# Kernel tuning notes

Hardware: AMD Instinct MI355X
Metric: run time of the kernel (lower is better)

Reference implementation:

```python
import jax, jax.numpy as jnp
import numpy as np

D_MODEL = 1024
N_HEADS = 16
D_FF = 4 * D_MODEL
EPS = 1e-5


def _layer_norm(x, g, b):
    mu = jnp.mean(x, axis=-1, keepdims=True)
    var = jnp.mean(jnp.square(x - mu), axis=-1, keepdims=True)
    return (x - mu) * jax.lax.rsqrt(var + EPS) * g + b


def _mha(x, Wq, Wk, Wv, Wo, causal):
    B, S, D = x.shape
    H = N_HEADS
    Dh = D // H
    q = (x @ Wq).reshape(B, S, H, Dh)
    k = (x @ Wk).reshape(B, S, H, Dh)
    v = (x @ Wv).reshape(B, S, H, Dh)
    scores = jnp.einsum('bqhd,bkhd->bhqk', q, k) / jnp.sqrt(jnp.asarray(Dh, x.dtype))
    if causal:
        mask = jnp.tril(jnp.ones((S, S), dtype=bool))  # [S,S] causal mask
        scores = jnp.where(mask, scores, jnp.asarray(-1e9, x.dtype))
    attn = jax.nn.softmax(scores, axis=-1)
    out = jnp.einsum('bhqk,bkhd->bqhd', attn, v).reshape(B, S, D)
    return out @ Wo


def _ffn(x, W1, b1, W2, b2):
    return jax.nn.relu(x @ W1 + b1) @ W2 + b2


def setup_inputs() -> dict:
    key = jax.random.key(0)
    ks = jax.random.split(key, 12)
    sd = 1.0 / np.sqrt(D_MODEL)
    sf = 1.0 / np.sqrt(D_FF)
    B, S = 4, 1024
    return {
        'X': jax.random.normal(ks[0], (B, S, D_MODEL), jnp.float32),
        'Wq1': jax.random.normal(ks[1], (D_MODEL, D_MODEL), jnp.float32) * sd,
        'Wk1': jax.random.normal(ks[2], (D_MODEL, D_MODEL), jnp.float32) * sd,
        'Wv1': jax.random.normal(ks[3], (D_MODEL, D_MODEL), jnp.float32) * sd,
        'Wo1': jax.random.normal(ks[4], (D_MODEL, D_MODEL), jnp.float32) * sd,
        'Wq2': jax.random.normal(ks[5], (D_MODEL, D_MODEL), jnp.float32) * sd,
        'Wk2': jax.random.normal(ks[6], (D_MODEL, D_MODEL), jnp.float32) * sd,
        'Wv2': jax.random.normal(ks[7], (D_MODEL, D_MODEL), jnp.float32) * sd,
        'Wo2': jax.random.normal(ks[8], (D_MODEL, D_MODEL), jnp.float32) * sd,
        'ln_g': jnp.ones((D_MODEL,), jnp.float32),
        'ln_b': jnp.zeros((D_MODEL,), jnp.float32),
        'W1': jax.random.normal(ks[9], (D_MODEL, D_FF), jnp.float32) * sd,
        'b1': jnp.zeros((D_FF,), jnp.float32),
        'W2': jax.random.normal(ks[10], (D_FF, D_MODEL), jnp.float32) * sf,
        'b2': jnp.zeros((D_MODEL,), jnp.float32),
    }


def reference(X, Wq1, Wk1, Wv1, Wo1, Wq2, Wk2, Wv2, Wo2, ln_g, ln_b, W1, b1, W2, b2):
    # Faithful to the torch module (including its unusual residual wiring
    # and the single shared LayerNorm used at all three sites).
    masked = _mha(X, Wq1, Wk1, Wv1, Wo1, causal=True)
    norm_masked = X + _layer_norm(masked, ln_g, ln_b)
    attn2 = _mha(norm_masked, Wq2, Wk2, Wv2, Wo2, causal=False)
    norm_attn2 = attn2 + _layer_norm(attn2, ln_g, ln_b)
    ff = _ffn(norm_attn2, W1, b1, W2, b2)
    return norm_attn2 + _layer_norm(ff, ln_g, ln_b)
```

## Files before the change

kernel.cpp:

```cpp
#include <hip/hip_runtime.h>
#include <hip/hip_bf16.h>

#define D_MODEL 1024
#define N_HEADS 16
#define DH 64
#define D_FF   4096
#define SEQ    1024
#define BATCH  4
#define TOK    (BATCH*SEQ)
#define EPS    1e-5f
#define SCALE  0.125f
#define QSCL   0.18033688f

typedef unsigned short USHORT;
typedef __attribute__((ext_vector_type(8))) short short8v;
typedef __attribute__((ext_vector_type(4))) float f32x4;

__device__ __forceinline__ USHORT f2bf(float f) {
    unsigned int u; __builtin_memcpy(&u, &f, 4);
    u += 0x7fffu + ((u >> 16) & 1u);
    return (USHORT)(u >> 16);
}
__device__ __forceinline__ USHORT f2bf_fast(float f) {
    unsigned int u; __builtin_memcpy(&u, &f, 4);
    return (USHORT)((u + 0x8000u) >> 16);
}
__device__ __forceinline__ unsigned pk2bf(float lo, float hi) {
    __hip_bfloat162 h = __float22bfloat162_rn(make_float2(lo, hi));
    unsigned u; __builtin_memcpy(&u, &h, 4);
    return u;
}
__device__ __forceinline__ float bf2f(USHORT s) {
    unsigned int u = ((unsigned int)s) << 16;
    float f; __builtin_memcpy(&f, &u, 4);
    return f;
}
__device__ __forceinline__ float max3f(float a, float b, float c) {
    return fmaxf(fmaxf(a, b), c);
}
__device__ __forceinline__ float fexp2(float x) {
#if __has_builtin(__builtin_amdgcn_exp2f)
    return __builtin_amdgcn_exp2f(x);
#else
    return exp2f(x);
#endif
}

__device__ __forceinline__ short8v ld_frag(const USHORT* lds, int row, int c8) {
    return *reinterpret_cast<const short8v*>(
        &lds[row * 64 + (((c8) ^ (row & 7)) << 3)]);
}

#define GLDS(gsrc, ldst) \
    __builtin_amdgcn_global_load_lds( \
        (const __attribute__((address_space(1))) void*)(gsrc), \
        (__attribute__((address_space(3))) void*)(ldst), 16, 0, 0)

#define WAITVM(n) asm volatile("s_waitcnt vmcnt(" #n ")" ::: "memory")

__global__ __launch_bounds__(512) void gemm_k256p8_kernel(
    const USHORT* __restrict__ A, const USHORT* __restrict__ Bt,
    float* __restrict__ Cf, USHORT* __restrict__ Cb, USHORT* __restrict__ Ck,
    USHORT* __restrict__ VtOut,
    int M, int N, int K, const float* __restrict__ bias, int relu, int qkv)
{
    __shared__ USHORT smem[65536];

    const int tid = threadIdx.x;
    const int l   = tid & 63;
    const int w   = tid >> 6;
    const int wr  = w >> 2, wc = w & 3;
    const int lr  = l & 15, lg = l >> 4;

    const int gx  = gridDim.x;
    const int nwg = gx * gridDim.y;
    const int lin = blockIdx.y * gx + blockIdx.x;
    const int swz = (lin & 7) * (nwg >> 3) + (lin >> 3);
    const int m0  = (swz / gx) * 256, n0 = (swz % gx) * 256;

    const int srow = tid >> 3;
    const int scol = ((tid & 7) ^ (srow & 7)) << 3;
    const USHORT* aS0 = A  + (size_t)(m0 + srow) * K + scol;
    const USHORT* bS0 = Bt + (size_t)(n0 + srow) * K + scol;
    const int dof0 = (w * 64) * 8;
    const int dof1 = (512 + w * 64) * 8;

    auto stageH = [&](int mat, int d, int h, int koff) {
        const USHORT* src = (mat ? bS0 : aS0) + (size_t)(h * 128) * K + koff;
        USHORT* dst = smem + mat * 32768 + d * 16384 + h * 8192;
        GLDS(src, dst + dof0);
        GLDS(src + (size_t)64 * K, dst + dof1);
    };

    f32x4 acc[8][4];
#pragma unroll
    for (int i = 0; i < 8; ++i)
#pragma unroll
        for (int j = 0; j < 4; ++j) acc[i][j] = (f32x4){0.f, 0.f, 0.f, 0.f};

    const int nk = K >> 6;

    stageH(0, 0, 0, 0);  stageH(0, 0, 1, 0);
    stageH(1, 0, 0, 0);  stageH(1, 0, 1, 0);
    stageH(1, 1, 0, 64); stageH(1, 1, 1, 64);

    for (int kt = 0; kt < nk; ++kt) {
        const int d = kt & 1;
        const USHORT* Ah = smem + d * 16384 + wr * 8192;
        const USHORT* Bh = smem + 32768 + d * 16384 + (wc >> 1) * 8192;
        const int brow = (wc & 1) * 64;
        short8v bfr[4][2];

#pragma unroll
        for (int g = 0; g < 4; ++g) {
            if (g == 0) {
                if (kt + 1 < nk) { WAITVM(4); } else { WAITVM(0); }
            }
            __builtin_amdgcn_s_barrier();

            if (g == 0) {
#pragma unroll
                for (int ni = 0; ni < 4; ++ni) {
                    bfr[ni][0] = ld_frag(Bh, brow + ni * 16 + lr, lg);
                    bfr[ni][1] = ld_frag(Bh, brow + ni * 16 + lr, 4 + lg);
                }
            }
            short8v a0k0 = ld_frag(Ah, (g * 2) * 16 + lr, lg);
            short8v a0k1 = ld_frag(Ah, (g * 2) * 16 + lr, 4 + lg);
            short8v a1k0 = ld_frag(Ah, (g * 2 + 1) * 16 + lr, lg);
            short8v a1k1 = ld_frag(Ah, (g * 2 + 1) * 16 + lr, 4 + lg);

            if (g == 0 && kt + 1 < nk) stageH(0, (kt + 1) & 1, 0, (kt + 1) * 64);
            if (g == 1 && kt + 1 < nk) stageH(0, (kt + 1) & 1, 1, (kt + 1) * 64);
            if (g == 2 && kt + 2 < nk) stageH(1, kt & 1, 0, (kt + 2) * 64);
            if (g == 3 && kt + 2 < nk) stageH(1, kt & 1, 1, (kt + 2) * 64);

            __builtin_amdgcn_s_setprio(1);
#pragma unroll
            for (int ni = 0; ni < 4; ++ni) {
                acc[g * 2][ni] = __builtin_amdgcn_mfma_f32_16x16x32_bf16(
                    a0k0, bfr[ni][0], acc[g * 2][ni], 0, 0, 0);
                acc[g * 2][ni] = __builtin_amdgcn_mfma_f32_16x16x32_bf16(
                    a0k1, bfr[ni][1], acc[g * 2][ni], 0, 0, 0);
                acc[g * 2 + 1][ni] = __builtin_amdgcn_mfma_f32_16x16x32_bf16(
                    a1k0, bfr[ni][0], acc[g * 2 + 1][ni], 0, 0, 0);
                acc[g * 2 + 1][ni] = __builtin_amdgcn_mfma_f32_16x16x32_bf16(
                    a1k1, bfr[ni][1], acc[g * 2 + 1][ni], 0, 0, 0);
            }
            __builtin_amdgcn_s_setprio(0);
        }
    }

    if (qkv) {
#pragma unroll
        for (int mi = 0; mi < 8; ++mi) {
            const int row = m0 + wr * 128 + mi * 16 + (l >> 4) * 4;
#pragma unroll
            for (int ni = 0; ni < 4; ++ni) {
                const int col = n0 + wc * 64 + ni * 16 + lr;
                if (col < 2048) {
                    USHORT* dst = (col < 1024) ? Cb : Ck;
                    const float scl = (col < 1024) ? QSCL : 1.f;
                    const int c = col & 1023;
#pragma unroll
                    for (int j = 0; j < 4; ++j)
                        dst[(size_t)(row + j) * D_MODEL + c] =
                            f2bf(acc[mi][ni][j] * scl);
                } else {
                    const int c = col - 2048;
                    const int bb = row >> 10, jr = row & 1023;
                    const int hh = c >> 6, dd = c & 63;
                    uint2 pk = make_uint2(
                        pk2bf(acc[mi][ni][0], acc[mi][ni][1]),
                        pk2bf(acc[mi][ni][2], acc[mi][ni][3]));
                    *reinterpret_cast<uint2*>(
                        &VtOut[((size_t)(bb * 16 + hh) * 64 + dd) * 1024 + jr]) = pk;
                }
            }
        }
    } else {
#pragma unroll
        for (int mi = 0; mi < 8; ++mi) {
            const int row = m0 + wr * 128 + mi * 16 + (l >> 4) * 4;
#pragma unroll
            for (int ni = 0; ni < 4; ++ni) {
                const int col = n0 + wc * 64 + ni * 16 + lr;
                const float bv = bias ? bias[col] : 0.f;
#pragma unroll
                for (int j = 0; j < 4; ++j) {
                    float v = acc[mi][ni][j] + bv;
                    if (relu) v = fmaxf(v, 0.f);
                    const size_t idx = (size_t)(row + j) * N + col;
                    if (Cf) Cf[idx] = v;
                    if (Cb) Cb[idx] = f2bf(v);
                }
            }
        }
    }
}

__global__ __launch_bounds__(512) void gemm_k256p8s4_kernel(
    const USHORT* __restrict__ A, const USHORT* __restrict__ Bt,
    USHORT* __restrict__ Pa, USHORT* __restrict__ Pb,
    USHORT* __restrict__ Pc, USHORT* __restrict__ Pd,
    int M, int N, int K)
{
    __shared__ USHORT smem[65536];

    const int tid = threadIdx.x;
    const int l   = tid & 63;
    const int w   = tid >> 6;
    const int wr  = w >> 2, wc = w & 3;
    const int lr  = l & 15, lg = l >> 4;

    const int gx  = gridDim.x;
    const int nwg = gx * gridDim.y;
    const int lin = blockIdx.y * gx + blockIdx.x;
    const int swz = (lin & 7) * (nwg >> 3) + (lin >> 3);
    const int my  = swz / gx;
    const int mt  = M >> 8;
    const int part = my / mt;
    const int m0  = (my % mt) << 8;
    const int n0  = (swz % gx) * 256;
    const int koff = part * (K >> 2);
    USHORT* dst = (part == 0) ? Pa : (part == 1) ? Pb : (part == 2) ? Pc : Pd;

    const int srow = tid >> 3;
    const int scol = ((tid & 7) ^ (srow & 7)) << 3;
    const USHORT* aS0 = A  + (size_t)(m0 + srow) * K + scol;
    const USHORT* bS0 = Bt + (size_t)(n0 + srow) * K + scol;
    const int dof0 = (w * 64) * 8;
    const int dof1 = (512 + w * 64) * 8;

    auto stageH = [&](int mat, int d, int h, int ko) {
        const USHORT* src = (mat ? bS0 : aS0) + (size_t)(h * 128) * K + ko;
        USHORT* dst2 = smem + mat * 32768 + d * 16384 + h * 8192;
        GLDS(src, dst2 + dof0);
        GLDS(src + (size_t)64 * K, dst2 + dof1);
    };

    f32x4 acc[8][4];
#pragma unroll
    for (int i = 0; i < 8; ++i)
#pragma unroll
        for (int j = 0; j < 4; ++j) acc[i][j] = (f32x4){0.f, 0.f, 0.f, 0.f};

    const int nk = K >> 8;

    stageH(0, 0, 0, koff);      stageH(0, 0, 1, koff);
    stageH(1, 0, 0, koff);      stageH(1, 0, 1, koff);
    stageH(1, 1, 0, koff + 64); stageH(1, 1, 1, koff + 64);

    for (int kt = 0; kt < nk; ++kt) {
        const int d = kt & 1;
        const USHORT* Ah = smem + d * 16384 + wr * 8192;
        const USHORT* Bh = smem + 32768 + d * 16384 + (wc >> 1) * 8192;
        const int brow = (wc & 1) * 64;
        short8v bfr[4][2];

#pragma unroll
        for (int g = 0; g < 4; ++g) {
            if (g == 0) {
                if (kt + 1 < nk) { WAITVM(4); } else { WAITVM(0); }
            }
            __builtin_amdgcn_s_barrier();

            if (g == 0) {
#pragma unroll
                for (int ni = 0; ni < 4; ++ni) {
                    bfr[ni][0] = ld_frag(Bh, brow + ni * 16 + lr, lg);
                    bfr[ni][1] = ld_frag(Bh, brow + ni * 16 + lr, 4 + lg);
                }
            }
            short8v a0k0 = ld_frag(Ah, (g * 2) * 16 + lr, lg);
            short8v a0k1 = ld_frag(Ah, (g * 2) * 16 + lr, 4 + lg);
            short8v a1k0 = ld_frag(Ah, (g * 2 + 1) * 16 + lr, lg);
            short8v a1k1 = ld_frag(Ah, (g * 2 + 1) * 16 + lr, 4 + lg);

            if (g == 0 && kt + 1 < nk) stageH(0, (kt + 1) & 1, 0, koff + (kt + 1) * 64);
            if (g == 1 && kt + 1 < nk) stageH(0, (kt + 1) & 1, 1, koff + (kt + 1) * 64);
            if (g == 2 && kt + 2 < nk) stageH(1, kt & 1, 0, koff + (kt + 2) * 64);
            if (g == 3 && kt + 2 < nk) stageH(1, kt & 1, 1, koff + (kt + 2) * 64);

            __builtin_amdgcn_s_setprio(1);
#pragma unroll
            for (int ni = 0; ni < 4; ++ni) {
                acc[g * 2][ni] = __builtin_amdgcn_mfma_f32_16x16x32_bf16(
                    a0k0, bfr[ni][0], acc[g * 2][ni], 0, 0, 0);
                acc[g * 2][ni] = __builtin_amdgcn_mfma_f32_16x16x32_bf16(
                    a0k1, bfr[ni][1], acc[g * 2][ni], 0, 0, 0);
                acc[g * 2 + 1][ni] = __builtin_amdgcn_mfma_f32_16x16x32_bf16(
                    a1k0, bfr[ni][0], acc[g * 2 + 1][ni], 0, 0, 0);
                acc[g * 2 + 1][ni] = __builtin_amdgcn_mfma_f32_16x16x32_bf16(
                    a1k1, bfr[ni][1], acc[g * 2 + 1][ni], 0, 0, 0);
            }
            __builtin_amdgcn_s_setprio(0);
        }
    }

#pragma unroll
    for (int mi = 0; mi < 8; ++mi) {
        const int row = m0 + wr * 128 + mi * 16 + (l >> 4) * 4;
#pragma unroll
        for (int ni = 0; ni < 4; ++ni) {
            const int col = n0 + wc * 64 + ni * 16 + lr;
#pragma unroll
            for (int j = 0; j < 4; ++j)
                dst[(size_t)(row + j) * N + col] = f2bf(acc[mi][ni][j]);
        }
    }
}

__global__ __launch_bounds__(512) void gemm_k128c_kernel(
    const USHORT* __restrict__ A, const USHORT* __restrict__ Bt,
    USHORT* __restrict__ Pa, USHORT* __restrict__ Pb,
    int M, int N, int K)
{
    __shared__ USHORT As[2][128 * 64];
    __shared__ USHORT Bs[2][128 * 64];

    const int tid = threadIdx.x;
    const int l   = tid & 63;
    const int w   = tid >> 6;
    const int wr  = w >> 2, wc = w & 3;
    const int lr  = l & 15, lg = l >> 4;

    const int gx  = gridDim.x;
    const int nwg = gx * gridDim.y;
    const int lin = blockIdx.y * gx + blockIdx.x;
    const int swz = (lin & 7) * (nwg >> 3) + (lin >> 3);
    const int my  = swz / gx;
    const int mt  = M >> 7;
    const int part = my / mt;
    const int m0  = (my % mt) << 7;
    const int n0  = (swz % gx) * 128;
    const int koff = part * (K >> 1);
    USHORT* dst = part ? Pb : Pa;

    const USHORT* aS[2]; const USHORT* bS[2]; int dOf[2];
#pragma unroll
    for (int p = 0; p < 2; ++p) {
        const int q = p * 512 + tid;
        const int row = q >> 3, cu = q & 7;
        const int cs = ((cu ^ (row & 7)) << 3);
        aS[p] = A  + (size_t)(m0 + row) * K + cs;
        bS[p] = Bt + (size_t)(n0 + row) * K + cs;
        dOf[p] = (p * 512 + w * 64) * 8;
    }

    auto stage = [&](int buf, int k0) {
#pragma unroll
        for (int p = 0; p < 2; ++p) {
            GLDS(aS[p] + k0, &As[buf][dOf[p]]);
            GLDS(bS[p] + k0, &Bs[buf][dOf[p]]);
        }
    };

    f32x4 acc[4][2];
#pragma unroll
    for (int i = 0; i < 4; ++i)
#pragma unroll
        for (int j = 0; j < 2; ++j) acc[i][j] = (f32x4){0.f, 0.f, 0.f, 0.f};

    const int nk = K >> 7;
    stage(0, koff);

    for (int t = 0; t < nk; ++t) {
        const int cur = t & 1;
        if (t + 1 < nk) {
            stage(cur ^ 1, koff + ((t + 1) << 6));
            WAITVM(4);
        } else {
            WAITVM(0);
        }
        __builtin_amdgcn_s_barrier();

#pragma unroll
        for (int ks = 0; ks < 2; ++ks) {
            short8v bfr[2];
#pragma unroll
            for (int ni = 0; ni < 2; ++ni)
                bfr[ni] = ld_frag(Bs[cur], wc * 32 + ni * 16 + lr, ks * 4 + lg);
            __builtin_amdgcn_s_setprio(1);
#pragma unroll
            for (int mi = 0; mi < 4; ++mi) {
                short8v af = ld_frag(As[cur], wr * 64 + mi * 16 + lr, ks * 4 + lg);
#pragma unroll
                for (int ni = 0; ni < 2; ++ni)
                    acc[mi][ni] = __builtin_amdgcn_mfma_f32_16x16x32_bf16(
                        af, bfr[ni], acc[mi][ni], 0, 0, 0);
            }
            __builtin_amdgcn_s_setprio(0);
        }
        __builtin_amdgcn_s_barrier();
    }

#pragma unroll
    for (int mi = 0; mi < 4; ++mi) {
        const int row = m0 + wr * 64 + mi * 16 + (l >> 4) * 4;
#pragma unroll
        for (int ni = 0; ni < 2; ++ni) {
            const int col = n0 + wc * 32 + ni * 16 + lr;
#pragma unroll
            for (int j = 0; j < 4; ++j)
                dst[(size_t)(row + j) * N + col] = f2bf(acc[mi][ni][j]);
        }
    }
}

struct TcvtB4 {
    const float* s0; const float* s1; const float* s2; const float* s3;
    USHORT* d0; USHORT* d1; USHORT* d2; USHORT* d3;
};

__device__ __forceinline__ void tcvt_body(
    const float* __restrict__ W, USHORT* __restrict__ Wt, int K, int N)
{
    __shared__ USHORT L[64][65];
    const int tid = threadIdx.x;
    const int tx = tid & 15, ty = tid >> 4;
    const int n0 = blockIdx.x * 64, k0 = blockIdx.y * 64;
#pragma unroll
    for (int r = 0; r < 4; ++r) {
        int kr = ty + 16 * r;
        float4 v = *reinterpret_cast<const float4*>(
            &W[(size_t)(k0 + kr) * N + n0 + tx * 4]);
        L[tx * 4 + 0][kr] = f2bf(v.x);
        L[tx * 4 + 1][kr] = f2bf(v.y);
        L[tx * 4 + 2][kr] = f2bf(v.z);
        L[tx * 4 + 3][kr] = f2bf(v.w);
    }
    __syncthreads();
#pragma unroll
    for (int r = 0; r < 4; ++r) {
        int nr = ty + 16 * r;
        ushort4 o = make_ushort4(L[nr][tx * 4 + 0], L[nr][tx * 4 + 1],
                                 L[nr][tx * 4 + 2], L[nr][tx * 4 + 3]);
        *reinterpret_cast<ushort4*>(&Wt[(size_t)(n0 + nr) * K + k0 + tx * 4]) = o;
    }
}

__global__ __launch_bounds__(256) void tcvt_kernel(
    const float* __restrict__ W, USHORT* __restrict__ Wt, int K, int N)
{
    tcvt_body(W, Wt, K, N);
}

__global__ __launch_bounds__(256) void tcvt4_kernel(TcvtB4 p, int K, int N)
{
    const int z = blockIdx.z;
    const float* W = (z == 0) ? p.s0 : (z == 1) ? p.s1 : (z == 2) ? p.s2 : p.s3;
    USHORT*    Wt = (z == 0) ? p.d0 : (z == 1) ? p.d1 : (z == 2) ? p.d2 : p.d3;
    tcvt_body(W, Wt, K, N);
}

__global__ __launch_bounds__(256) void f2b_kernel(
    const float* __restrict__ in, USHORT* __restrict__ out, int n4)
{
    int i = blockIdx.x * 256 + threadIdx.x;
    if (i < n4) {
        float4 v = reinterpret_cast<const float4*>(in)[i];
        reinterpret_cast<ushort4*>(out)[i] =
            make_ushort4(f2bf(v.x), f2bf(v.y), f2bf(v.z), f2bf(v.w));
    }
}

__global__ __launch_bounds__(256) void attn_mfma_kernel(
    const USHORT* __restrict__ Q, const USHORT* __restrict__ K,
    const USHORT* __restrict__ Vt, USHORT* __restrict__ O, int causal)
{
    __shared__ USHORT smem[20480];

    const int tid = threadIdx.x;
    const int l  = tid & 63;
    const int w  = tid >> 6;
    const int lr = l & 15;
    const int lg = l >> 4;

    const int lin = blockIdx.y * 16 + blockIdx.x;
    const int swz = (lin & 7) * 128 + (lin >> 3);
    const int qtr = swz & 15;
    const int qt  = causal ? (qtr ^ (((swz >> 5) & 1) ? 15 : 0)) : qtr;
    const int bh = swz >> 4;
    const int h = bh & 15, b = bh >> 4;
    const int q0 = qt * 64;

    const USHORT* gq  = Q  + (size_t)(b * SEQ + q0) * D_MODEL + h * DH;
    const USHORT* gk0 = K  + (size_t)b * SEQ * D_MODEL + h * DH;
    const USHORT* gv0 = Vt + (size_t)bh * DH * SEQ;

    auto stageK = [&](int buf, int kt) {
        USHORT* dst = smem + buf * 4096;
        const size_t base = (size_t)kt * 64 * 1024;
#pragma unroll
        for (int p = 0; p < 2; ++p) {
            const int q = p * 256 + tid;
            const int row = q >> 3, cu = q & 7;
            GLDS(gk0 + base + (size_t)row * 1024 + ((cu ^ (row & 7)) << 3),
                 dst + (p * 256 + w * 64) * 8);
        }
    };
    auto stageV = [&](int buf, int kt) {
        USHORT* dst = smem + 8192 + buf * 4096;
        const int j0 = kt * 64;
#pragma unroll
        for (int p = 0; p < 2; ++p) {
            const int q = p * 256 + tid;
            const int row = q >> 3, cu = q & 7;
            GLDS(gv0 + (size_t)row * 1024 + j0 + ((cu ^ (row & 7)) << 3),
                 dst + (p * 256 + w * 64) * 8);
        }
    };

#pragma unroll
    for (int p = 0; p < 2; ++p) {
        const int q = p * 256 + tid;
        const int row = q >> 3, cu = q & 7;
        GLDS(gq + (size_t)row * 1024 + ((cu ^ (row & 7)) << 3),
             smem + 16384 + (p * 256 + w * 64) * 8);
    }
    stageK(0, 0);
    stageV(0, 0);

    f32x4 oacc[4];
    float m_ = -1e30f, l_ = 0.f;
#pragma unroll
    for (int d = 0; d < 4; ++d) oacc[d] = (f32x4){0.f, 0.f, 0.f, 0.f};

    int paddr[4];
#pragma unroll
    for (int jb = 0; jb < 4; ++jb) {
        const int cu = jb * 2 + (lg >> 1);
        paddr[jb] = lr * 64 + ((cu ^ (lr & 7)) << 3) + (lg & 1) * 4;
    }

    __syncthreads();
    short8v qa0 = ld_frag(smem + 16384, w * 16 + lr, lg);
    short8v qa1 = ld_frag(smem + 16384, w * 16 + lr, 4 + lg);
    __syncthreads();
    USHORT* PsW = smem + 16384 + w * 1024;

    const int ntile = causal ? (qt + 1) : (SEQ / 64);
    for (int kt = 0; kt < ntile; ++kt) {
        const int cur = kt & 1;
        if (kt + 1 < ntile) {
            stageK(cur ^ 1, kt + 1);
            stageV(cur ^ 1, kt + 1);
        }
        const int j0 = kt * 64;
        const USHORT* KsC = smem + cur * 4096;
        const USHORT* VsC = smem + 8192 + cur * 4096;

        f32x4 sa[4];
        __builtin_amdgcn_s_setprio(1);
#pragma unroll
        for (int jb = 0; jb < 4; ++jb) {
            short8v kf0 = ld_frag(KsC, jb * 16 + lr, lg);
            short8v kf1 = ld_frag(KsC, jb * 16 + lr, 4 + lg);
            sa[jb] = (f32x4){0.f, 0.f, 0.f, 0.f};
            sa[jb] = __builtin_amdgcn_mfma_f32_16x16x32_bf16(
                kf0, qa0, sa[jb], 0, 0, 0);
            sa[jb] = __builtin_amdgcn_mfma_f32_16x16x32_bf16(
                kf1, qa1, sa[jb], 0, 0, 0);
        }
        __builtin_amdgcn_s_setprio(0);

        if (causal && kt >= ntile - 1) {
            const int qrow = q0 + w * 16 + lr;
#pragma unroll
            for (int jb = 0; jb < 4; ++jb)
#pragma unroll
                for (int r = 0; r < 4; ++r)
                    if ((j0 + jb * 16 + lg * 4 + r) > qrow)
                        sa[jb][r] = -1e30f;
        }

        float t1 = max3f(sa[0][0], sa[0][1], sa[0][2]);
        float t2 = max3f(sa[0][3], sa[1][0], sa[1][1]);
        float t3 = max3f(sa[1][2], sa[1][3], sa[2][0]);
        float t4 = max3f(sa[2][1], sa[2][2], sa[2][3]);
        float t5 = max3f(sa[3][0], sa[3][1], sa[3][2]);
        float tm = fmaxf(max3f(max3f(t1, t2, t3), t4, t5), sa[3][3]);
        tm = fmaxf(tm, __shfl_xor(tm, 16));
        tm = fmaxf(tm, __shfl_xor(tm, 32));

        const bool anyf = (tm > m_ + 8.f);
        if (__ballot(anyf)) {
            const float mn = anyf ? tm : m_;
            const float sc = fexp2(m_ - mn);
            l_ *= sc;
            m_ = mn;
#pragma unroll
            for (int r = 0; r < 4; ++r) {
                const float scr = __shfl(sc, (l & 48) | (lg * 4 + r));
#pragma unroll
                for (int d = 0; d < 4; ++d) oacc[d][r] *= scr;
            }
        }

#pragma unroll
        for (int jb = 0; jb < 4; ++jb) {
            const float p0 = fexp2(sa[jb][0] - m_);
            const float p1 = fexp2(sa[jb][1] - m_);
            const float p2 = fexp2(sa[jb][2] - m_);
            const float p3 = fexp2(sa[jb][3] - m_);
            l_ += (p0 + p1) + (p2 + p3);
            *reinterpret_cast<uint2*>(&PsW[paddr[jb]]) =
                make_uint2(pk2bf(p0, p1), pk2bf(p2, p3));
        }

        __builtin_amdgcn_s_setprio(1);
#pragma unroll
        for (int ks = 0; ks < 2; ++ks) {
            short8v pa = ld_frag(PsW, lr, ks * 4 + lg);
#pragma unroll
            for (int d = 0; d < 4; ++d) {
                short8v vf = ld_frag(VsC, d * 16 + lr, ks * 4 + lg);
                oacc[d] = __builtin_amdgcn_mfma_f32_16x16x32_bf16(
                    pa, vf, oacc[d], 0, 0, 0);
            }
        }
        __builtin_amdgcn_s_setprio(0);
        __syncthreads();
    }

    USHORT* go = O + (size_t)(b * SEQ + q0 + w * 16) * D_MODEL + h * DH;
    float lv = l_;
    lv += __shfl_xor(lv, 16);
    lv += __shfl_xor(lv, 32);
    const float inv_own = 1.f / lv;
#pragma unroll
    for (int r = 0; r < 4; ++r) {
        const float inv = __shfl(inv_own, (l & 48) | (lg * 4 + r));
        const int qrow = lg * 4 + r;
#pragma unroll
        for (int d = 0; d < 4; ++d)
            go[(size_t)qrow * D_MODEL + d * 16 + lr] =
                f2bf_fast(oacc[d][r] * inv);
    }
}

__global__ __launch_bounds__(256) void ln_res_kernel(
    const USHORT* __restrict__ xb, const USHORT* __restrict__ xb2,
    const USHORT* __restrict__ xb3, const USHORT* __restrict__ xb4,
    const float* __restrict__ biasx,
    const float* __restrict__ resf, const USHORT* __restrict__ resb,
    const float* __restrict__ g, const float* __restrict__ bta,
    float* __restrict__ outf, USHORT* __restrict__ outb)
{
    __shared__ float red[256];
    __shared__ float s_mu, s_rstd;

    const int row = blockIdx.x;
    const int tid = threadIdx.x;
    ushort4 xv = reinterpret_cast<const ushort4*>(xb + (size_t)row * D_MODEL)[tid];
    float vx = bf2f(xv.x), vy = bf2f(xv.y), vz = bf2f(xv.z), vw = bf2f(xv.w);
    if (xb2) {
        ushort4 x2 = reinterpret_cast<const ushort4*>(
            xb2 + (size_t)row * D_MODEL)[tid];
        vx += bf2f(x2.x); vy += bf2f(x2.y); vz += bf2f(x2.z); vw += bf2f(x2.w);
    }
    if (xb3) {
        ushort4 x3 = reinterpret_cast<const ushort4*>(
            xb3 + (size_t)row * D_MODEL)[tid];
        vx += bf2f(x3.x); vy += bf2f(x3.y); vz += bf2f(x3.z); vw += bf2f(x3.w);
    }
    if (xb4) {
        ushort4 x4 = reinterpret_cast<const ushort4*>(
            xb4 + (size_t)row * D_MODEL)[tid];
        vx += bf2f(x4.x); vy += bf2f(x4.y); vz += bf2f(x4.z); vw += bf2f(x4.w);
    }
    if (biasx) {
        float4 bx = reinterpret_cast<const float4*>(biasx)[tid];
        vx += bx.x; vy += bx.y; vz += bx.z; vw += bx.w;
    }

    red[tid] = vx + vy + vz + vw;
    __syncthreads();
    for (int s = 128; s > 0; s >>= 1) {
        if (tid < s) red[tid] += red[tid + s];
        __syncthreads();
    }
    if (tid == 0) s_mu = red[0] * (1.f / D_MODEL);
    __syncthreads();
    const float mu = s_mu;

    float dx = vx - mu, dy = vy - mu, dz = vz - mu, dw = vw - mu;
    red[tid] = dx * dx + dy * dy + dz * dz + dw * dw;
    __syncthreads();
    for (int s = 128; s > 0; s >>= 1) {
        if (tid < s) red[tid] += red[tid + s];
        __syncthreads();
    }
    if (tid == 0) s_rstd = rsqrtf(red[0] * (1.f / D_MODEL) + EPS);
    __syncthreads();
    const float rstd = s_rstd;

    float4 rv;
    if (resf) {
        rv = reinterpret_cast<const float4*>(resf + (size_t)row * D_MODEL)[tid];
    } else if (resb) {
        ushort4 rb = reinterpret_cast<const ushort4*>(
            resb + (size_t)row * D_MODEL)[tid];
        rv = make_float4(bf2f(rb.x), bf2f(rb.y), bf2f(rb.z), bf2f(rb.w));
    } else {
        rv = make_float4(vx, vy, vz, vw);
    }
    float4 gv = reinterpret_cast<const float4*>(g)[tid];
    float4 bv = reinterpret_cast<const float4*>(bta)[tid];

    float4 o;
    o.x = rv.x + dx * rstd * gv.x + bv.x;
    o.y = rv.y + dy * rstd * gv.y + bv.y;
    o.z = rv.z + dz * rstd * gv.z + bv.z;
    o.w = rv.w + dw * rstd * gv.w + bv.w;
    reinterpret_cast<float4*>(outf + (size_t)row * D_MODEL)[tid] = o;
    if (outb)
        reinterpret_cast<ushort4*>(outb + (size_t)row * D_MODEL)[tid] =
            make_ushort4(f2bf(o.x), f2bf(o.y), f2bf(o.z), f2bf(o.w));
}

extern "C" void kernel_launch(void* const* d_in, const int* in_sizes, int n_in,
                              void* d_out, int out_size, void* d_ws, size_t ws_size,
                              hipStream_t stream)
{
    const float* X    = (const float*)d_in[0];
    const float* Wq1  = (const float*)d_in[1];
    const float* Wk1  = (const float*)d_in[2];
    const float* Wv1  = (const float*)d_in[3];
    const float* Wo1  = (const float*)d_in[4];
    const float* Wq2  = (const float*)d_in[5];
    const float* Wk2  = (const float*)d_in[6];
    const float* Wv2  = (const float*)d_in[7];
    const float* Wo2  = (const float*)d_in[8];
    const float* ln_g = (const float*)d_in[9];
    const float* ln_b = (const float*)d_in[10];
    const float* W1   = (const float*)d_in[11];
    const float* b1   = (const float*)d_in[12];
    const float* W2   = (const float*)d_in[13];
    const float* b2   = (const float*)d_in[14];

    const size_t MI = 1024 * 1024;
    USHORT* ws16 = (USHORT*)d_ws;
    USHORT* Wqkv1t = ws16;
    USHORT* scr0   = ws16;
    USHORT* Wo1t   = ws16 + 3 * MI;
    USHORT* Wqkv2t = ws16 + 4 * MI;
    USHORT* Wo2t   = ws16 + 7 * MI;
    USHORT* W2t    = ws16 + 8 * MI;
    USHORT* Xb     = ws16 + 12 * MI;
    USHORT* W1t    = Xb;
    USHORT* qb     = ws16 + 16 * MI;
    USHORT* kb     = ws16 + 20 * MI;
    USHORT* Vtb    = ws16 + 24 * MI;
    USHORT* t0b    = ws16 + 28 * MI;
    USHORT* hb     = qb;
    USHORT* t2b    = ws16 + 32 * MI;
    USHORT* t1b    = ws16 + 36 * MI;
    float*  t2     = (float*)(ws16 + 40 * MI);

    auto gemmBig = [&](const USHORT* A, const USHORT* Bt, float* Cf, USHORT* Cb,
                       int M, int N, int K, const float* bias, int relu) {
        gemm_k256p8_kernel<<<dim3(N / 256, M / 256), 512, 0, stream>>>(
            A, Bt, Cf, Cb, nullptr, nullptr, M, N, K, bias, relu, 0);
    };
    auto gemm_qkv = [&](const USHORT* A, const USHORT* Bt) {
        gemm_k256p8_kernel<<<dim3(3072 / 256, TOK / 256), 512, 0, stream>>>(
            A, Bt, nullptr, qb, kb, Vtb, TOK, 3072, D_MODEL, nullptr, 0, 1);
    };
    auto gemm128c = [&](const USHORT* A, const USHORT* Bt, USHORT* Pa, USHORT* Pb,
                        int M, int N, int K) {
        gemm_k128c_kernel<<<dim3(N / 128, (M / 128) * 2), 512, 0, stream>>>(
            A, Bt, Pa, Pb, M, N, K);
    };
    auto gemm256s4 = [&](const USHORT* A, const USHORT* Bt,
                         USHORT* Pa, USHORT* Pb, USHORT* Pc, USHORT* Pd,
                         int M, int N, int K) {
        gemm_k256p8s4_kernel<<<dim3(N / 256, (M / 256) * 4), 512, 0, stream>>>(
            A, Bt, Pa, Pb, Pc, Pd, M, N, K);
    };

    dim3 agrid(SEQ / 64, BATCH * N_HEADS);

    {
        TcvtB4 p1{Wq1, Wk1, Wv1, Wo1,
                  Wqkv1t, Wqkv1t + 1 * MI, Wqkv1t + 2 * MI, Wo1t};
        tcvt4_kernel<<<dim3(16, 16, 4), 256, 0, stream>>>(p1, D_MODEL, D_MODEL);
        TcvtB4 p2{Wq2, Wk2, Wv2, Wo2,
                  Wqkv2t, Wqkv2t + 1 * MI, Wqkv2t + 2 * MI, Wo2t};
        tcvt4_kernel<<<dim3(16, 16, 4), 256, 0, stream>>>(p2, D_MODEL, D_MODEL);
    }
    tcvt_kernel<<<dim3(D_MODEL / 64, D_FF / 64), 256, 0, stream>>>(
        W2, W2t, D_FF, D_MODEL);
    f2b_kernel<<<dim3(4096), 256, 0, stream>>>(X, Xb, TOK * D_MODEL / 4);

    gemm_qkv(Xb, Wqkv1t);
    attn_mfma_kernel<<<agrid, 256, 0, stream>>>(qb, kb, Vtb, t0b, 1);
    gemm128c(t0b, Wo1t, t2b, t1b, TOK, D_MODEL, D_MODEL);
    ln_res_kernel<<<dim3(TOK), 256, 0, stream>>>(t2b, t1b, nullptr, nullptr,
                                                 nullptr, X, nullptr,
                                                 ln_g, ln_b, t2, t2b);
    tcvt_kernel<<<dim3(D_FF / 64, D_MODEL / 64), 256, 0, stream>>>(
        W1, W1t, D_MODEL, D_FF);

    gemm_qkv(t2b, Wqkv2t);
    attn_mfma_kernel<<<agrid, 256, 0, stream>>>(qb, kb, Vtb, t0b, 0);
    gemm128c(t0b, Wo2t, scr0, t1b, TOK, D_MODEL, D_MODEL);
    ln_res_kernel<<<dim3(TOK), 256, 0, stream>>>(scr0, t1b, nullptr, nullptr,
                                                 nullptr, nullptr, nullptr,
                                                 ln_g, ln_b, t2, t2b);

    gemmBig(t2b, W1t, nullptr, hb, TOK, D_FF, D_MODEL, b1, 1);
    gemm256s4(hb, W2t, scr0, W1t, t2b, t1b, TOK, D_MODEL, D_FF);
    ln_res_kernel<<<dim3(TOK), 256, 0, stream>>>(scr0, W1t, t2b, t1b, b2,
                                                 t2, nullptr,
                                                 ln_g, ln_b, (float*)d_out, nullptr);
}
```

Measured before the change: 299.7 us.

## Software-pipeline LDS fragment loads ahead of MFMA in GEMM main loops

Restructures the inner k-loop of two GEMM kernels so the A/B register fragments for the next sub-step are loaded from LDS after the current MFMA batch has been issued. The first fragments are preloaded before the loop, and the next tile's fragments are fetched at the end of the last group. The aim is to hide LDS read latency behind MFMA execution instead of stalling at the start of each group. Barrier and vmcnt wait placement changes to match. This shifts the synchronization ordering, which carries a risk of LDS races, and adds register pressure.

```diff
diff --git a/kernel.cpp b/kernel.cpp
--- a/kernel.cpp
+++ b/kernel.cpp
@@ -58,6 +58,8 @@
 
 #define WAITVM(n) asm volatile("s_waitcnt vmcnt(" #n ")" ::: "memory")
 
+#define MFMA_BF16 __builtin_amdgcn_mfma_f32_16x16x32_bf16
+
 __global__ __launch_bounds__(512) void gemm_k256p8_kernel(
     const USHORT* __restrict__ A, const USHORT* __restrict__ Bt,
     float* __restrict__ Cf, USHORT* __restrict__ Cb, USHORT* __restrict__ Ck,
@@ -99,55 +101,72 @@
         for (int j = 0; j < 4; ++j) acc[i][j] = (f32x4){0.f, 0.f, 0.f, 0.f};
 
     const int nk = K >> 6;
+    const int brow = (wc & 1) * 64;
 
     stageH(0, 0, 0, 0);  stageH(0, 0, 1, 0);
     stageH(1, 0, 0, 0);  stageH(1, 0, 1, 0);
     stageH(1, 1, 0, 64); stageH(1, 1, 1, 64);
+    WAITVM(4);
+    __builtin_amdgcn_s_barrier();
+
+    short8v bfr[4][2];
+    short8v afr[2][2];
+    {
+        const USHORT* Ah = smem + wr * 8192;
+        const USHORT* Bh = smem + 32768 + (wc >> 1) * 8192;
+#pragma unroll
+        for (int ni = 0; ni < 4; ++ni) {
+            bfr[ni][0] = ld_frag(Bh, brow + ni * 16 + lr, lg);
+            bfr[ni][1] = ld_frag(Bh, brow + ni * 16 + lr, 4 + lg);
+        }
+        afr[0][0] = ld_frag(Ah, 0 + lr, lg);
+        afr[0][1] = ld_frag(Ah, 0 + lr, 4 + lg);
+        afr[1][0] = ld_frag(Ah, 16 + lr, lg);
+        afr[1][1] = ld_frag(Ah, 16 + lr, 4 + lg);
+    }
 
     for (int kt = 0; kt < nk; ++kt) {
         const int d = kt & 1;
         const USHORT* Ah = smem + d * 16384 + wr * 8192;
-        const USHORT* Bh = smem + 32768 + d * 16384 + (wc >> 1) * 8192;
-        const int brow = (wc & 1) * 64;
-        short8v bfr[4][2];
 
 #pragma unroll
         for (int g = 0; g < 4; ++g) {
-            if (g == 0) {
-                if (kt + 1 < nk) { WAITVM(4); } else { WAITVM(0); }
+            __builtin_amdgcn_s_setprio(1);
+#pragma unroll
+            for (int ni = 0; ni < 4; ++ni) {
+                acc[g * 2][ni]     = MFMA_BF16(afr[0][0], bfr[ni][0], acc[g * 2][ni], 0, 0, 0);
+                acc[g * 2][ni]     = MFMA_BF16(afr[0][1], bfr[ni][1], acc[g * 2][ni], 0, 0, 0);
+                acc[g * 2 + 1][ni] = MFMA_BF16(afr[1][0], bfr[ni][0], acc[g * 2 + 1][ni], 0, 0, 0);
+                acc[g * 2 + 1][ni] = MFMA_BF16(afr[1][1], bfr[ni][1], acc[g * 2 + 1][ni], 0, 0, 0);
             }
-            __builtin_amdgcn_s_barrier();
-
-            if (g == 0) {
-#pragma unroll
-                for (int ni = 0; ni < 4; ++ni) {
-                    bfr[ni][0] = ld_frag(Bh, brow + ni * 16 + lr, lg);
-                    bfr[ni][1] = ld_frag(Bh, brow + ni * 16 + lr, 4 + lg);
-                }
-            }
-            short8v a0k0 = ld_frag(Ah, (g * 2) * 16 + lr, lg);
-            short8v a0k1 = ld_frag(Ah, (g * 2) * 16 + lr, 4 + lg);
-            short8v a1k0 = ld_frag(Ah, (g * 2 + 1) * 16 + lr, lg);
-            short8v a1k1 = ld_frag(Ah, (g * 2 + 1) * 16 + lr, 4 + lg);
+            __builtin_amdgcn_s_setprio(0);
 
             if (g == 0 && kt + 1 < nk) stageH(0, (kt + 1) & 1, 0, (kt + 1) * 64);
             if (g == 1 && kt + 1 < nk) stageH(0, (kt + 1) & 1, 1, (kt + 1) * 64);
-            if (g == 2 && kt + 2 < nk) stageH(1, kt & 1, 0, (kt + 2) * 64);
-            if (g == 3 && kt + 2 < nk) stageH(1, kt & 1, 1, (kt + 2) * 64);
-
-            __builtin_amdgcn_s_setprio(1);
-#pragma unroll
-            for (int ni = 0; ni < 4; ++ni) {
-                acc[g * 2][ni] = __builtin_amdgcn_mfma_f32_16x16x32_bf16(
-                    a0k0, bfr[ni][0], acc[g * 2][ni], 0, 0, 0);
-                acc[g * 2][ni] = __builtin_amdgcn_mfma_f32_16x16x32_bf16(
-                    a0k1, bfr[ni][1], acc[g * 2][ni], 0, 0, 0);
-                acc[g * 2 + 1][ni] = __builtin_amdgcn_mfma_f32_16x16x32_bf16(
-                    a1k0, bfr[ni][0], acc[g * 2 + 1][ni], 0, 0, 0);
-                acc[g * 2 + 1][ni] = __builtin_amdgcn_mfma_f32_16x16x32_bf16(
-                    a1k1, bfr[ni][1], acc[g * 2 + 1][ni], 0, 0, 0);
+            if (g == 2 && kt + 2 < nk) stageH(1, d, 0, (kt + 2) * 64);
+            if (g == 3 && kt + 2 < nk) stageH(1, d, 1, (kt + 2) * 64);
+
+            if (g < 3) {
+                afr[0][0] = ld_frag(Ah, (g * 2 + 2) * 16 + lr, lg);
+                afr[0][1] = ld_frag(Ah, (g * 2 + 2) * 16 + lr, 4 + lg);
+                afr[1][0] = ld_frag(Ah, (g * 2 + 3) * 16 + lr, lg);
+                afr[1][1] = ld_frag(Ah, (g * 2 + 3) * 16 + lr, 4 + lg);
+                __builtin_amdgcn_s_barrier();
+            } else if (kt + 1 < nk) {
+                if (kt + 2 < nk) { WAITVM(4); } else { WAITVM(0); }
+                __builtin_amdgcn_s_barrier();
+                const USHORT* Ah2 = smem + (d ^ 1) * 16384 + wr * 8192;
+                const USHORT* Bh2 = smem + 32768 + (d ^ 1) * 16384 + (wc >> 1) * 8192;
+#pragma unroll
+                for (int ni = 0; ni < 4; ++ni) {
+                    bfr[ni][0] = ld_frag(Bh2, brow + ni * 16 + lr, lg);
+                    bfr[ni][1] = ld_frag(Bh2, brow + ni * 16 + lr, 4 + lg);
+                }
+                afr[0][0] = ld_frag(Ah2, 0 + lr, lg);
+                afr[0][1] = ld_frag(Ah2, 0 + lr, 4 + lg);
+                afr[1][0] = ld_frag(Ah2, 16 + lr, lg);
+                afr[1][1] = ld_frag(Ah2, 16 + lr, 4 + lg);
             }
-            __builtin_amdgcn_s_setprio(0);
         }
     }
 
@@ -246,55 +265,72 @@
         for (int j = 0; j < 4; ++j) acc[i][j] = (f32x4){0.f, 0.f, 0.f, 0.f};
 
     const int nk = K >> 8;
+    const int brow = (wc & 1) * 64;
 
     stageH(0, 0, 0, koff);      stageH(0, 0, 1, koff);
     stageH(1, 0, 0, koff);      stageH(1, 0, 1, koff);
     stageH(1, 1, 0, koff + 64); stageH(1, 1, 1, koff + 64);
+    WAITVM(4);
+    __builtin_amdgcn_s_barrier();
+
+    short8v bfr[4][2];
+    short8v afr[2][2];
+    {
+        const USHORT* Ah = smem + wr * 8192;
+        const USHORT* Bh = smem + 32768 + (wc >> 1) * 8192;
+#pragma unroll
+        for (int ni = 0; ni < 4; ++ni) {
+            bfr[ni][0] = ld_frag(Bh, brow + ni * 16 + lr, lg);
+            bfr[ni][1] = ld_frag(Bh, brow + ni * 16 + lr, 4 + lg);
+        }
+        afr[0][0] = ld_frag(Ah, 0 + lr, lg);
+        afr[0][1] = ld_frag(Ah, 0 + lr, 4 + lg);
+        afr[1][0] = ld_frag(Ah, 16 + lr, lg);
+        afr[1][1] = ld_frag(Ah, 16 + lr, 4 + lg);
+    }
 
     for (int kt = 0; kt < nk; ++kt) {
         const int d = kt & 1;
         const USHORT* Ah = smem + d * 16384 + wr * 8192;
-        const USHORT* Bh = smem + 32768 + d * 16384 + (wc >> 1) * 8192;
-        const int brow = (wc & 1) * 64;
-        short8v bfr[4][2];
 
 #pragma unroll
         for (int g = 0; g < 4; ++g) {
-            if (g == 0) {
-                if (kt + 1 < nk) { WAITVM(4); } else { WAITVM(0); }
+            __builtin_amdgcn_s_setprio(1);
+#pragma unroll
+            for (int ni = 0; ni < 4; ++ni) {
+                acc[g * 2][ni]     = MFMA_BF16(afr[0][0], bfr[ni][0], acc[g * 2][ni], 0, 0, 0);
+                acc[g * 2][ni]     = MFMA_BF16(afr[0][1], bfr[ni][1], acc[g * 2][ni], 0, 0, 0);
+                acc[g * 2 + 1][ni] = MFMA_BF16(afr[1][0], bfr[ni][0], acc[g * 2 + 1][ni], 0, 0, 0);
+                acc[g * 2 + 1][ni] = MFMA_BF16(afr[1][1], bfr[ni][1], acc[g * 2 + 1][ni], 0, 0, 0);
             }
-            __builtin_amdgcn_s_barrier();
-
-            if (g == 0) {
-#pragma unroll
-                for (int ni = 0; ni < 4; ++ni) {
-                    bfr[ni][0] = ld_frag(Bh, brow + ni * 16 + lr, lg);
-                    bfr[ni][1] = ld_frag(Bh, brow + ni * 16 + lr, 4 + lg);
-                }
-            }
-            short8v a0k0 = ld_frag(Ah, (g * 2) * 16 + lr, lg);
-            short8v a0k1 = ld_frag(Ah, (g * 2) * 16 + lr, 4 + lg);
-            short8v a1k0 = ld_frag(Ah, (g * 2 + 1) * 16 + lr, lg);
-            short8v a1k1 = ld_frag(Ah, (g * 2 + 1) * 16 + lr, 4 + lg);
+            __builtin_amdgcn_s_setprio(0);
 
             if (g == 0 && kt + 1 < nk) stageH(0, (kt + 1) & 1, 0, koff + (kt + 1) * 64);
             if (g == 1 && kt + 1 < nk) stageH(0, (kt + 1) & 1, 1, koff + (kt + 1) * 64);
-            if (g == 2 && kt + 2 < nk) stageH(1, kt & 1, 0, koff + (kt + 2) * 64);
-            if (g == 3 && kt + 2 < nk) stageH(1, kt & 1, 1, koff + (kt + 2) * 64);
-
-            __builtin_amdgcn_s_setprio(1);
-#pragma unroll
-            for (int ni = 0; ni < 4; ++ni) {
-                acc[g * 2][ni] = __builtin_amdgcn_mfma_f32_16x16x32_bf16(
-                    a0k0, bfr[ni][0], acc[g * 2][ni], 0, 0, 0);
-                acc[g * 2][ni] = __builtin_amdgcn_mfma_f32_16x16x32_bf16(
-                    a0k1, bfr[ni][1], acc[g * 2][ni], 0, 0, 0);
-                acc[g * 2 + 1][ni] = __builtin_amdgcn_mfma_f32_16x16x32_bf16(
-                    a1k0, bfr[ni][0], acc[g * 2 + 1][ni], 0, 0, 0);
-                acc[g * 2 + 1][ni] = __builtin_amdgcn_mfma_f32_16x16x32_bf16(
-                    a1k1, bfr[ni][1], acc[g * 2 + 1][ni], 0, 0, 0);
+            if (g == 2 && kt + 2 < nk) stageH(1, d, 0, koff + (kt + 2) * 64);
+            if (g == 3 && kt + 2 < nk) stageH(1, d, 1, koff + (kt + 2) * 64);
+
+            if (g < 3) {
+                afr[0][0] = ld_frag(Ah, (g * 2 + 2) * 16 + lr, lg);
+                afr[0][1] = ld_frag(Ah, (g * 2 + 2) * 16 + lr, 4 + lg);
+                afr[1][0] = ld_frag(Ah, (g * 2 + 3) * 16 + lr, lg);
+                afr[1][1] = ld_frag(Ah, (g * 2 + 3) * 16 + lr, 4 + lg);
+                __builtin_amdgcn_s_barrier();
+            } else if (kt + 1 < nk) {
+                if (kt + 2 < nk) { WAITVM(4); } else { WAITVM(0); }
+                __builtin_amdgcn_s_barrier();
+                const USHORT* Ah2 = smem + (d ^ 1) * 16384 + wr * 8192;
+                const USHORT* Bh2 = smem + 32768 + (d ^ 1) * 16384 + (wc >> 1) * 8192;
+#pragma unroll
+                for (int ni = 0; ni < 4; ++ni) {
+                    bfr[ni][0] = ld_frag(Bh2, brow + ni * 16 + lr, lg);
+                    bfr[ni][1] = ld_frag(Bh2, brow + ni * 16 + lr, 4 + lg);
+                }
+                afr[0][0] = ld_frag(Ah2, 0 + lr, lg);
+                afr[0][1] = ld_frag(Ah2, 0 + lr, 4 + lg);
+                afr[1][0] = ld_frag(Ah2, 16 + lr, lg);
+                afr[1][1] = ld_frag(Ah2, 16 + lr, 4 + lg);
             }
-            __builtin_amdgcn_s_setprio(0);
         }
     }
 
```

New measurement: 300.6 us. About the same (+0.3%).
